# Performance work log

Hardware: AMD Instinct MI355X
Metric: run time of the kernel (lower is better)

The kernel has to match this reference:

```python
import jax, jax.numpy as jnp
import numpy as np

# lct_fk config (matches init_kwargs)
BIN_LEN = 0.01
WALL_SIZE = 2.0
C_LIGHT = 3.0e8


def _safe_sqrt(v):
    # sqrt(relu(v)) with a well-defined (zero) subgradient at v<=0
    pos = v > 0
    return jnp.where(pos, jnp.sqrt(jnp.where(pos, v, 1.0)), 0.0)


def _trilinear_zero(vol, pz, py, px):
    # vol: (D,H,W) complex64; pz/py/px: (D2,H2,W2) float pixel coords
    # Trilinear sampling with zeros padding (== F.grid_sample align_corners=False)
    D, H, W = vol.shape
    z0f = jnp.floor(pz); y0f = jnp.floor(py); x0f = jnp.floor(px)
    dz = pz - z0f; dy = py - y0f; dx = px - x0f
    z0 = z0f.astype(jnp.int32); y0 = y0f.astype(jnp.int32); x0 = x0f.astype(jnp.int32)
    out = jnp.zeros(pz.shape, vol.dtype)
    for iz, wz in ((z0, 1.0 - dz), (z0 + 1, dz)):
        for iy, wy in ((y0, 1.0 - dy), (y0 + 1, dy)):
            for ix, wx in ((x0, 1.0 - dx), (x0 + 1, dx)):
                valid = (iz >= 0) & (iz < D) & (iy >= 0) & (iy < H) & (ix >= 0) & (ix < W)
                v = vol[jnp.clip(iz, 0, D - 1), jnp.clip(iy, 0, H - 1), jnp.clip(ix, 0, W - 1)]
                w = jnp.where(valid, wz * wy * wx, 0.0)
                out = out + w * v
    return out


def setup_inputs() -> dict:
    key = jax.random.key(0)
    feture = jax.random.uniform(key, (1, 2, 128, 128, 128), dtype=jnp.float32)
    return {"feture_bxdxtxhxw": feture}


def reference(feture_bxdxtxhxw):
    b, d, T, H, W = feture_bxdxtxhxw.shape
    M, N = T, H  # temprol_grid (== crop), sptial_grid; tbes=0, tens=crop -> no temporal pad
    width = WALL_SIZE / 2.0
    trange = M * BIN_LEN  # crop * c * (bin_len/c)

    # z-weighting: (z/(M-1))^2, then sqrt(relu(.))
    gridz = (jnp.arange(M, dtype=jnp.float32) / (M - 1)).reshape(1, M, 1, 1)
    data = feture_bxdxtxhxw.reshape(b * d, T, H, W) * (gridz ** 2)
    data = _safe_sqrt(jax.nn.relu(data))

    # zero-pad to (2T,2H,2W), FFT, fftshift (roll by half == fftshift for even sizes)
    datapad = jnp.pad(data, ((0, 0), (0, M), (0, N), (0, N)))
    fre = jnp.fft.fftshift(jnp.fft.fftn(datapad, axes=(-3, -2, -1)), axes=(-3, -2, -1))

    # Stolt (f-k) warped coordinates, normalized to [-1,1]
    zdim = (jnp.arange(2 * M, dtype=jnp.float32) - M) / M
    xdim = (jnp.arange(2 * N, dtype=jnp.float32) - N) / N
    gz = zdim[:, None, None]            # varies along axis 0
    gy = xdim[None, :, None]            # varies along axis 1
    gx = xdim[None, None, :]            # varies along axis 2
    fk = (N * trange / (M * width * 4.0)) ** 2
    gznew = jnp.sqrt(fk * (gx ** 2 + gy ** 2) + gz ** 2)  # (2M,2N,2N)
    gznew = jnp.broadcast_to(gznew, (2 * M, 2 * N, 2 * N))

    # unnormalize (align_corners=False): pix = ((c+1)*size - 1)/2
    px = ((jnp.broadcast_to(gx, gznew.shape) + 1.0) * (2 * N) - 1.0) * 0.5
    py = ((jnp.broadcast_to(gy, gznew.shape) + 1.0) * (2 * N) - 1.0) * 0.5
    pz = ((gznew + 1.0) * (2 * M) - 1.0) * 0.5

    samp = jax.vmap(lambda v: _trilinear_zero(v, pz, py, px))(fre)

    # zero negative/zero frequencies along z, then Stolt Jacobian scaling
    z0pos = M + 1  # first index where zdim > 0
    zmask = (jnp.arange(2 * M) >= z0pos)[None, :, None, None]
    samp = samp * zmask
    samp = samp * (jnp.abs(gz) / (gznew + 1e-8))[None]

    samp = jnp.fft.fftshift(samp, axes=(-3, -2, -1))  # ifftshift == fftshift (even dims)
    vol = jnp.fft.ifftn(samp, axes=(-3, -2, -1))
    out = vol[:, :M, :N, :N].real
    return out.reshape(b, d, M, N, N)
```

## Files before the change

kernel.cpp:

```cpp
#include <hip/hip_runtime.h>

static constexpr size_t VS   = 8388608;
static constexpr int    ZSTR = 65536;
static constexpr int    YSTR = 256;
static constexpr size_t VSB  = 4194304;
static constexpr int    BZS  = 32768;
static constexpr int    BYS  = 128;
static constexpr int    LSTR = 261;

typedef float vf2 __attribute__((ext_vector_type(2)));

__device__ __forceinline__ vf2 cmul(vf2 a, vf2 b){
    vf2 asw; asw.x = -a.y; asw.y = a.x;
    return a*b.x + asw*b.y;
}

constexpr int BREV(int k){ return ((k&1)<<3)|((k&2)<<1)|((k&4)>>1)|((k&8)>>3); }

__device__ __forceinline__ void bf(vf2& a, vf2& b, float c, float s){
    vf2 sum = a + b;
    vf2 dif = a - b;
    vf2 dsw; dsw.x = -dif.y; dsw.y = dif.x;
    b = dif*c + dsw*s;
    a = sum;
}

template<int DIR>
__device__ __forceinline__ void fft16(vf2 r[16]){
    constexpr float D = (float)DIR;
    constexpr float C16[8] = {1.f, 0.92387953f, 0.70710678f, 0.38268343f, 0.f, -0.38268343f, -0.70710678f, -0.92387953f};
    constexpr float S16[8] = {0.f, 0.38268343f, 0.70710678f, 0.92387953f, 1.f, 0.92387953f, 0.70710678f, 0.38268343f};
#pragma unroll
    for (int j = 0; j < 8; ++j) bf(r[j], r[j+8], C16[j], D*S16[j]);
    constexpr float C8[4] = {1.f, 0.70710678f, 0.f, -0.70710678f};
    constexpr float S8[4] = {0.f, 0.70710678f, 1.f, 0.70710678f};
#pragma unroll
    for (int g = 0; g < 16; g += 8)
#pragma unroll
        for (int j = 0; j < 4; ++j) bf(r[g+j], r[g+j+4], C8[j], D*S8[j]);
#pragma unroll
    for (int g = 0; g < 16; g += 4){
        bf(r[g],   r[g+2], 1.f, 0.f);
        bf(r[g+1], r[g+3], 0.f, D);
    }
#pragma unroll
    for (int g = 0; g < 16; g += 2) bf(r[g], r[g+1], 1.f, 0.f);
}

__device__ __forceinline__ void init_tw(vf2* tw, float dir){
    int tid = threadIdx.x;
    float ang = dir * 0.0245436926f * (float)((tid >> 4)*(tid & 15));
    float s, c; __sincosf(ang, &s, &c);
    vf2 w; w.x = c; w.y = s;
    tw[tid] = w;
}

template<int DIR>
__device__ __forceinline__ void mid256s(vf2 r[16], vf2* sh8, const vf2* tw, int t, int l){
    fft16<DIR>(r);
#pragma unroll
    for (int k1 = 1; k1 < 16; ++k1)
        r[BREV(k1)] = cmul(r[BREV(k1)], tw[k1*16 + t]);
    int lr = l & 7;
    bool lo = (l < 8);
    __syncthreads();
    if (lo){
#pragma unroll
        for (int k1 = 0; k1 < 16; ++k1) sh8[lr*LSTR + k1*16 + (t ^ k1)] = r[BREV(k1)];
    }
    __syncthreads();
    if (lo){
#pragma unroll
        for (int n2 = 0; n2 < 16; ++n2) r[n2] = sh8[lr*LSTR + t*16 + (n2 ^ t)];
    }
    __syncthreads();
    if (!lo){
#pragma unroll
        for (int k1 = 0; k1 < 16; ++k1) sh8[lr*LSTR + k1*16 + (t ^ k1)] = r[BREV(k1)];
    }
    __syncthreads();
    if (!lo){
#pragma unroll
        for (int n2 = 0; n2 < 16; ++n2) r[n2] = sh8[lr*LSTR + t*16 + (n2 ^ t)];
    }
    fft16<DIR>(r);
}

template<int DIR, int NIN, int NOUT>
__device__ __forceinline__ void fft_strided(vf2* g, int S){
    __shared__ vf2 sh8[8*LSTR];
    __shared__ vf2 tw[256];
    int t = threadIdx.x >> 4, l = threadIdx.x & 15;
    vf2 r[16];
    vf2 zero; zero.x = 0.f; zero.y = 0.f;
#pragma unroll
    for (int n1 = 0; n1 < 16; ++n1)
        r[n1] = (n1 < NIN/16) ? g[(size_t)(16*n1 + t)*S + l] : zero;
    init_tw(tw, (float)DIR);
    __syncthreads();
    mid256s<DIR>(r, sh8, tw, t, l);
#pragma unroll
    for (int k2 = 0; k2 < 16; ++k2)
        if (k2 < NOUT/16) g[(size_t)(t + 16*k2)*S + l] = r[BREV(k2)];
}

__global__ void __launch_bounds__(256) k_p1(const float* __restrict__ in, vf2* __restrict__ A){
    __shared__ vf2 sh8[8*LSTR];
    __shared__ vf2 tw[256];
    __shared__ float shin[16*130];
    init_tw(tw, -1.f);
    int th = threadIdx.x, bid = blockIdx.x;
    int yc = bid & 7, z = (bid >> 3) & 127, v = bid >> 10;
    float gz = z * (1.0f/127.0f);
    float g2 = gz*gz;
    const float* src = in + (((size_t)(v*128 + z))*128 + yc*16)*128;
    for (int idx = th; idx < 2048; idx += 256){
        float val = src[idx] * g2;
        shin[(idx >> 7)*130 + (idx & 127)] = val > 0.f ? sqrtf(val) : 0.f;
    }
    __syncthreads();
    int t = th >> 4, l = th & 15;
    vf2 r[16];
    vf2 zero; zero.x = 0.f; zero.y = 0.f;
#pragma unroll
    for (int n1 = 0; n1 < 16; ++n1){
        r[n1] = zero;
        if (n1 < 8) r[n1].x = shin[l*130 + 16*n1 + t];
    }
    mid256s<-1>(r, sh8, tw, t, l);
    int lr = l & 7;
    vf2* dst = A + (size_t)v*VS + (size_t)z*ZSTR + (size_t)(yc*16)*YSTR;
#pragma unroll
    for (int half = 0; half < 2; ++half){
        __syncthreads();
        if ((l >> 3) == half){
#pragma unroll
            for (int k2 = 0; k2 < 16; ++k2) sh8[lr*LSTR + t + 16*k2] = r[BREV(k2)];
        }
        __syncthreads();
        vf2* d2 = dst + half*8*YSTR;
        for (int idx = th; idx < 2048; idx += 256){
            int line = idx >> 8, k = idx & 255;
            vf2 a = sh8[line*LSTR + k];
            vf2 p = sh8[line*LSTR + ((k - 1) & 255)];
            if (k == 128) p = zero;
            d2[idx] = (a + p)*0.5f;
        }
    }
}

__global__ void __launch_bounds__(256) k_p2z(vf2* __restrict__ A){
    int bid = blockIdx.x;
    int xb = bid & 15, y = (bid >> 4) & 127, v = bid >> 11;
    fft_strided<-1,128,128>(A + (size_t)v*VS + (size_t)y*YSTR + xb*16, ZSTR);
}

__global__ void __launch_bounds__(256) k_p3y(vf2* __restrict__ A){
    __shared__ vf2 sh8[8*LSTR];
    __shared__ vf2 tw[256];
    int bid = blockIdx.x;
    int xb = bid & 15, z = (bid >> 4) & 127, v = bid >> 11;
    vf2* g = A + (size_t)v*VS + (size_t)z*ZSTR + xb*16;
    int t = threadIdx.x >> 4, l = threadIdx.x & 15;
    vf2 r[16];
    vf2 zero; zero.x = 0.f; zero.y = 0.f;
#pragma unroll
    for (int n1 = 0; n1 < 16; ++n1)
        r[n1] = (n1 < 8) ? g[(size_t)(16*n1 + t)*YSTR + l] : zero;
    init_tw(tw, -1.f);
    __syncthreads();
    mid256s<-1>(r, sh8, tw, t, l);
    int lr = l & 7;
#pragma unroll
    for (int half = 0; half < 2; ++half){
        __syncthreads();
        if ((l >> 3) == half){
#pragma unroll
            for (int k2 = 0; k2 < 16; ++k2) sh8[lr*LSTR + t + 16*k2] = r[BREV(k2)];
        }
        __syncthreads();
        if ((l >> 3) == half){
#pragma unroll
            for (int k2 = 0; k2 < 16; ++k2){
                int k = t + 16*k2;
                vf2 a = sh8[lr*LSTR + k];
                vf2 p = sh8[lr*LSTR + ((k - 1) & 255)];
                if (k == 128) p = zero;
                g[(size_t)k*YSTR + l] = (a + p)*0.5f;
            }
        }
    }
}

__global__ void __launch_bounds__(256) k_p45(const vf2* __restrict__ A, vf2* __restrict__ B){
    __shared__ vf2 sh8[8*LSTR];
    __shared__ vf2 tw[256];
    init_tw(tw, 1.f);
    int tid = threadIdx.x, bid = blockIdx.x;
    int yc = bid & 15, zn = (bid >> 4) & 127, v = bid >> 11;
    const vf2* Av = A + (size_t)v*VS;
    int t = tid & 15, l = tid >> 4;
    int yn = yc*16 + l;
    float gy = (yn < 128 ? yn : yn - 256) * (1.0f/128.0f);
    float gz = zn * (1.0f/128.0f);
    float c2 = 0.1024f*gy*gy + gz*gz;
    unsigned rowoff = (unsigned)yn*YSTR;
    vf2 r[16];
#pragma unroll
    for (int n1 = 0; n1 < 16; ++n1){
        int xn = 16*n1 + t;
        float gx = (xn < 128 ? xn : xn - 256) * (1.0f/128.0f);
        float s2 = c2 + 0.1024f*gx*gx;
        float rs = __builtin_amdgcn_rsqf(s2 + 1e-12f);
        float gznew = s2 * rs;
        float pz = gznew*128.0f + 127.5f;
        int zi = (int)pz;
        float dz = pz - (float)zi;
        int zp0 = zi - 128;
        float wf = gz * rs;
        float w0 = (((unsigned)zp0     < 128u) ? (1.0f - dz) : 0.f) * wf;
        float w1 = (((unsigned)(zp0+1) < 128u) ? dz : 0.f) * wf;
        vf2 v0 = Av[(size_t)((unsigned)(zp0 & 127) * ZSTR) + rowoff + xn];
        vf2 v1 = Av[(size_t)((unsigned)((zp0 + 1) & 127) * ZSTR) + rowoff + xn];
        r[n1] = v0*w0 + v1*w1;
    }
    __syncthreads();
    mid256s<1>(r, sh8, tw, t, l);
    vf2* dst = B + (size_t)v*VSB + (size_t)zn*BZS + (size_t)yn*BYS;
#pragma unroll
    for (int k2 = 0; k2 < 8; ++k2)
        dst[t + 16*k2] = r[BREV(k2)];
}

__global__ void __launch_bounds__(256) k_p6(vf2* __restrict__ B){
    int bid = blockIdx.x;
    int xb = bid & 7, zn = (bid >> 3) & 127, v = bid >> 10;
    fft_strided<1,256,128>(B + (size_t)v*VSB + (size_t)zn*BZS + xb*16, BYS);
}

__global__ void __launch_bounds__(256) k_p7(const vf2* __restrict__ B, float* __restrict__ out){
    __shared__ vf2 sh8[8*LSTR];
    __shared__ vf2 tw[256];
    int bid = blockIdx.x;
    int xb = bid & 7, y = (bid >> 3) & 127, v = bid >> 10;
    const vf2* g = B + (size_t)v*VSB + (size_t)y*BYS + xb*16;
    int t = threadIdx.x >> 4, l = threadIdx.x & 15;
    vf2 r[16];
    vf2 zero; zero.x = 0.f; zero.y = 0.f;
#pragma unroll
    for (int n1 = 0; n1 < 16; ++n1)
        r[n1] = (n1 < 8) ? g[(size_t)(16*n1 + t)*BZS + l] : zero;
    init_tw(tw, 1.f);
    __syncthreads();
    mid256s<1>(r, sh8, tw, t, l);
    const float sc = 1.0f/16777216.0f;
    float* dst = out + ((size_t)(v*128)*128 + y)*128 + xb*16 + l;
#pragma unroll
    for (int k2 = 0; k2 < 8; ++k2)
        dst[(size_t)(t + 16*k2)*16384] = r[BREV(k2)].x * sc;
}

extern "C" void kernel_launch(void* const* d_in, const int* in_sizes, int n_in,
                              void* d_out, int out_size, void* d_ws, size_t ws_size,
                              hipStream_t stream){
    const float* in = (const float*)d_in[0];
    float* out = (float*)d_out;
    vf2* A = (vf2*)d_ws;
    vf2* B = A + 2*VS;
    k_p1 <<< 2048, 256, 0, stream>>>(in, A);
    k_p2z<<< 4096, 256, 0, stream>>>(A);
    k_p3y<<< 4096, 256, 0, stream>>>(A);
    k_p45<<< 4096, 256, 0, stream>>>(A, B);
    k_p6 <<< 2048, 256, 0, stream>>>(B);
    k_p7 <<< 2048, 256, 0, stream>>>(B, out);
}
```

Before: 198.2 us.

## Fold neighbor-averaging into pre-FFT twiddle in y-pass, drop shared-memory epilogue

The y-axis FFT kernel used to average each output with its neighbor through a two-pass shared-memory staging epilogue. That averaging is now applied as a per-input complex pre-multiplication by (1+e^{iθ})/2 before the FFT. The k=128 special case is handled by a separate alternating-sign sum reduced with wave shuffles. This removes the extra shared-memory round trips and barriers and writes results straight from registers, at the cost of sincos evaluations and a small reduction. Correctness depends on the shuffle and reduction indexing matching the thread layout.

```diff
diff --git a/kernel.cpp b/kernel.cpp
--- a/kernel.cpp
+++ b/kernel.cpp
@@ -158,6 +158,7 @@
 __global__ void __launch_bounds__(256) k_p3y(vf2* __restrict__ A){
     __shared__ vf2 sh8[8*LSTR];
     __shared__ vf2 tw[256];
+    __shared__ vf2 shW[64];
     int bid = blockIdx.x;
     int xb = bid & 15, z = (bid >> 4) & 127, v = bid >> 11;
     vf2* g = A + (size_t)v*VS + (size_t)z*ZSTR + xb*16;
@@ -167,29 +168,33 @@
 #pragma unroll
     for (int n1 = 0; n1 < 16; ++n1)
         r[n1] = (n1 < 8) ? g[(size_t)(16*n1 + t)*YSTR + l] : zero;
+
+    vf2 part = ((r[0]+r[1]) + (r[2]+r[3])) + ((r[4]+r[5]) + (r[6]+r[7]));
+    part = part * ((t & 1) ? -1.f : 1.f);
+    part.x += __shfl_xor(part.x, 16);
+    part.y += __shfl_xor(part.y, 16);
+    part.x += __shfl_xor(part.x, 32);
+    part.y += __shfl_xor(part.y, 32);
+    if ((t & 3) == 0) shW[(t >> 2)*16 + l] = part;
+
+#pragma unroll
+    for (int n1 = 0; n1 < 8; ++n1){
+        float sn, cn; __sincosf(0.0245436926f * (float)(16*n1 + t), &sn, &cn);
+        vf2 c; c.x = 0.5f*(1.f + cn); c.y = 0.5f*sn;
+        r[n1] = cmul(r[n1], c);
+    }
+
     init_tw(tw, -1.f);
     __syncthreads();
     mid256s<-1>(r, sh8, tw, t, l);
-    int lr = l & 7;
-#pragma unroll
-    for (int half = 0; half < 2; ++half){
-        __syncthreads();
-        if ((l >> 3) == half){
-#pragma unroll
-            for (int k2 = 0; k2 < 16; ++k2) sh8[lr*LSTR + t + 16*k2] = r[BREV(k2)];
-        }
-        __syncthreads();
-        if ((l >> 3) == half){
-#pragma unroll
-            for (int k2 = 0; k2 < 16; ++k2){
-                int k = t + 16*k2;
-                vf2 a = sh8[lr*LSTR + k];
-                vf2 p = sh8[lr*LSTR + ((k - 1) & 255)];
-                if (k == 128) p = zero;
-                g[(size_t)k*YSTR + l] = (a + p)*0.5f;
-            }
-        }
-    }
+
+    if (t == 0){
+        vf2 S = (shW[l] + shW[16 + l]) + (shW[32 + l] + shW[48 + l]);
+        r[BREV(8)] = S * 0.5f;
+    }
+#pragma unroll
+    for (int k2 = 0; k2 < 16; ++k2)
+        g[(size_t)(t + 16*k2)*YSTR + l] = r[BREV(k2)];
 }
 
 __global__ void __launch_bounds__(256) k_p45(const vf2* __restrict__ A, vf2* __restrict__ B){
```

Result: no change. 196.4 us (-0.9%).
